# Performance work log

Measured on AMD Instinct MI355X. Metric: run time of the kernel, lower is better.

The kernel has to match this reference:

```python
import jax, jax.numpy as jnp
import numpy as np

EPS = 1e-5

def _layernorm(x, g, b):
    m = jnp.mean(x, axis=-1, keepdims=True)
    v = jnp.var(x, axis=-1, keepdims=True)
    return (x - m) * jax.lax.rsqrt(v + EPS) * g + b

def setup_inputs() -> dict:
    key = jax.random.key(0)
    ks = jax.random.split(key, 8)
    B, N, D, H = 4, 2048, 1024, 16
    F = 2 * D
    s = 0.02
    return {
        "x": jax.random.normal(ks[0], (B, N, D), jnp.float32),
        "mask": jnp.zeros((B, N, N), jnp.float32),
        "Wq": jax.random.normal(ks[1], (D, D), jnp.float32) * s,
        "Wk": jax.random.normal(ks[2], (D, D), jnp.float32) * s,
        "Wv": jax.random.normal(ks[3], (D, D), jnp.float32) * s,
        "Wc": jax.random.normal(ks[4], (D, D), jnp.float32) * s,
        "bc": jnp.zeros((D,), jnp.float32),
        "W1": jax.random.normal(ks[5], (D, F), jnp.float32) * s,
        "b1": jnp.zeros((F,), jnp.float32),
        "W2": jax.random.normal(ks[6], (F, D), jnp.float32) * s,
        "b2": jnp.zeros((D,), jnp.float32),
        "g1": jnp.ones((D,), jnp.float32),
        "be1": jnp.zeros((D,), jnp.float32),
        "g2": jnp.ones((D,), jnp.float32),
        "be2": jnp.zeros((D,), jnp.float32),
    }

def reference(x, mask, Wq, Wk, Wv, Wc, bc, W1, b1, W2, b2, g1, be1, g2, be2):
    B, N, D = x.shape
    H = 16
    Dh = D // H
    scale = 1.0 / np.sqrt(Dh).astype(np.float32)
    # projections -> [B, H, N, Dh]
    def heads(t):
        return t.reshape(B, N, H, Dh).transpose(0, 2, 1, 3)
    q = heads(x @ Wq)
    k = heads(x @ Wk)
    v = heads(x @ Wv)
    score = jnp.einsum('bhnd,bhmd->bhnm', q, k) * scale + mask[:, None, :, :]
    attn = jnp.einsum('bhnm,bhmd->bhnd', jax.nn.softmax(score, axis=-1), v)
    attn = attn.transpose(0, 2, 1, 3).reshape(B, N, D)
    x = x + attn @ Wc + bc
    x = _layernorm(x, g1, be1)
    x = x + jnp.maximum(x @ W1 + b1, 0.0) @ W2 + b2
    x = _layernorm(x, g2, be2)
    return x
```

## Files before the change

kernel.cpp:

```cpp
#include <hip/hip_runtime.h>
#include <hip/hip_bf16.h>


#define DEV __device__ __forceinline__

using s16x8  = __attribute__((ext_vector_type(8))) short;
using f32x4  = __attribute__((ext_vector_type(4))) float;

DEV unsigned short f2bf(float f) {
  unsigned u = __float_as_uint(f);
  u += 0x7fffu + ((u >> 16) & 1u);
  return (unsigned short)(u >> 16);
}
DEV unsigned cvt_pk_bf16(float lo, float hi) {
  unsigned r;
  asm("v_cvt_pk_bf16_f32 %0, %1, %2" : "=v"(r) : "v"(lo), "v"(hi));
  return r;
}
DEV float bf2f(unsigned short b) { return __uint_as_float((unsigned)b << 16); }

typedef __attribute__((address_space(3))) unsigned lds_u32_t;
typedef const __attribute__((address_space(1))) unsigned glb_u32_t;

DEV void gld_lds16(const void* g, void* l) {
  __builtin_amdgcn_global_load_lds((glb_u32_t*)g, (lds_u32_t*)l, 16, 0, 0);
}

template<int RELU, int VOUT>
__global__ __launch_bounds__(512, 2)
void gemm8p(const unsigned short* __restrict__ A, const unsigned short* __restrict__ Bt,
            unsigned short* __restrict__ Cb, const float* __restrict__ bias,
            unsigned short* __restrict__ vtout, int M, int N, int K)
{
  __shared__ unsigned short Sh[2][2][256 * 64];
  const int tid = threadIdx.x;
  const int w = tid >> 6, lane = tid & 63;
  const int g = lane >> 4, q = lane & 15;
  const int wr = w >> 2, wc = w & 3;

  const int nwg  = gridDim.x * gridDim.y;
  const int flat = blockIdx.y * gridDim.x + blockIdx.x;
  const int rm   = (flat & 7) * (nwg >> 3) + (flat >> 3);
  const int m0 = (rm / gridDim.x) * 256, n0 = (rm % gridDim.x) * 256;

  f32x4 acc[8][4] = {};

  const int srow = w * 8 + (lane >> 3);
  const int scol = ((lane & 7) ^ (lane >> 3)) * 8;
  const unsigned short* Ag = A  + (size_t)(m0 + srow) * K + scol;
  const unsigned short* Bg = Bt + (size_t)(n0 + srow) * K + scol;

  auto STG = [&](const unsigned short* Gb, int buf, int ab, int half, int kt) {
    const unsigned short* gs = Gb + (size_t)(half * 128) * K + kt * 64;
    unsigned short* ls = &Sh[buf][ab][(half * 128 + w * 8) * 64];
    gld_lds16(gs, ls);
    gld_lds16(gs + (size_t)64 * K, ls + 64 * 64);
  };
  auto LDA = [&](int buf, int mq, s16x8 af[4][2]) {
#pragma unroll
    for (int mm = 0; mm < 4; ++mm) {
      const unsigned short* rp = &Sh[buf][0][(wr * 128 + mq * 64 + mm * 16 + q) * 64];
#pragma unroll
      for (int kk = 0; kk < 2; ++kk)
        af[mm][kk] = *(const s16x8*)(rp + (((kk * 4 + g) ^ (q & 7)) * 8));
    }
  };
  auto LDB = [&](int buf, int nq, s16x8 bf[2][2]) {
#pragma unroll
    for (int nn = 0; nn < 2; ++nn) {
      const unsigned short* rp = &Sh[buf][1][(wc * 64 + nq * 32 + nn * 16 + q) * 64];
#pragma unroll
      for (int kk = 0; kk < 2; ++kk)
        bf[nn][kk] = *(const s16x8*)(rp + (((kk * 4 + g) ^ (q & 7)) * 8));
    }
  };
  auto MQ = [&](int mq, int nq, const s16x8 af[4][2], const s16x8 bf[2][2]) {
    __builtin_amdgcn_s_setprio(1);
#pragma unroll
    for (int kk = 0; kk < 2; ++kk)
#pragma unroll
      for (int mm = 0; mm < 4; ++mm)
#pragma unroll
        for (int nn = 0; nn < 2; ++nn)
          acc[mq * 4 + mm][nq * 2 + nn] = __builtin_amdgcn_mfma_f32_16x16x32_bf16(
              af[mm][kk], bf[nn][kk], acc[mq * 4 + mm][nq * 2 + nn], 0, 0, 0);
    __builtin_amdgcn_s_setprio(0);
  };
  auto BAR = [&]() { __builtin_amdgcn_sched_barrier(0); __builtin_amdgcn_s_barrier(); };

  STG(Ag, 0, 0, 0, 0); STG(Ag, 0, 0, 1, 0);
  STG(Bg, 0, 1, 0, 0); STG(Bg, 0, 1, 1, 0);

  const int NKT = K >> 6;
  s16x8 af[4][2], bf0[2][2], bf1[2][2];
#pragma unroll 1
  for (int kt = 0; kt < NKT; ++kt) {
    const int b = kt & 1, sb = b ^ 1, kn = kt + 1;
    const bool stg = (kn < NKT);
    if (stg) { STG(Ag, sb, 0, 0, kn); asm volatile("s_waitcnt vmcnt(2)" ::: "memory"); }
    else     {                        asm volatile("s_waitcnt vmcnt(0)" ::: "memory"); }
    BAR();
    LDA(b, 0, af); LDB(b, 0, bf0);
    MQ(0, 0, af, bf0);
    BAR();
    if (stg) STG(Ag, sb, 0, 1, kn);
    LDB(b, 1, bf1);
    MQ(0, 1, af, bf1);
    BAR();
    if (stg) STG(Bg, sb, 1, 0, kn);
    LDA(b, 1, af);
    MQ(1, 0, af, bf0);
    BAR();
    if (stg) STG(Bg, sb, 1, 1, kn);
    MQ(1, 1, af, bf1);
    BAR();
  }

#pragma unroll
  for (int n = 0; n < 4; ++n) {
    const int col = n0 + wc * 64 + n * 16 + q;
    if (VOUT && col >= 2048) {
      const int cv = col - 2048;
#pragma unroll
      for (int m = 0; m < 8; ++m) {
        const int row0 = m0 + wr * 128 + m * 16 + g * 4;
        const int bb = row0 >> 11;
        ushort4 pk;
        pk.x = f2bf(acc[m][n][0]); pk.y = f2bf(acc[m][n][1]);
        pk.z = f2bf(acc[m][n][2]); pk.w = f2bf(acc[m][n][3]);
        *(ushort4*)(vtout + ((size_t)bb * 1024 + cv) * 2048 + (row0 & 2047)) = pk;
      }
    } else {
      const float scl = (VOUT && col < 1024) ? 0.18033688011112042f : 1.0f;
      const float bv = bias ? bias[col] : 0.0f;
#pragma unroll
      for (int m = 0; m < 8; ++m) {
        const int row0 = m0 + wr * 128 + m * 16 + g * 4;
#pragma unroll
        for (int r = 0; r < 4; ++r) {
          float v = acc[m][n][r] * scl + bv;
          if (RELU) v = fmaxf(v, 0.0f);
          Cb[(size_t)(row0 + r) * N + col] = f2bf(v);
        }
      }
    }
  }
}

template<int RELU, int RESID, int OUTF>
__global__ __launch_bounds__(256)
void gemm_bt(const unsigned short* __restrict__ A, const unsigned short* __restrict__ Bt,
             unsigned short* __restrict__ Cb, float* __restrict__ Cf,
             const float* __restrict__ bias, const float* __restrict__ resid,
             const unsigned short* __restrict__ residb,
             int M, int N, int K)
{
  __shared__ unsigned short As[2][4096];
  __shared__ unsigned short Bs[2][4096];
  const int tid  = threadIdx.x;
  const int wave = tid >> 6, lane = tid & 63;
  const int g = lane >> 4, q = lane & 15;

  const int nwg  = gridDim.x * gridDim.y;
  const int flat = blockIdx.y * gridDim.x + blockIdx.x;
  const int rm   = (nwg & 7) ? flat : ((flat & 7) * (nwg >> 3) + (flat >> 3));
  const int m0 = (rm / gridDim.x) * 128, n0 = (rm % gridDim.x) * 128;
  const int wr = wave >> 1, wc = wave & 1;

  f32x4 acc[4][4] = {};

  const int i0 = wave * 512 + lane * 8;
  const int i1 = 2048 + i0;

  auto STAGE = [&](int buf, int kt) {
    gld_lds16(A  + (size_t)(m0 + (i0 >> 5)) * K + kt + (i0 & 31), As[buf] + wave * 512);
    gld_lds16(Bt + (size_t)(n0 + (i0 >> 5)) * K + kt + (i0 & 31), Bs[buf] + wave * 512);
    gld_lds16(A  + (size_t)(m0 + (i1 >> 5)) * K + kt + (i1 & 31), As[buf] + 2048 + wave * 512);
    gld_lds16(Bt + (size_t)(n0 + (i1 >> 5)) * K + kt + (i1 & 31), Bs[buf] + 2048 + wave * 512);
  };

  STAGE(0, 0);
  __syncthreads();
  int cur = 0;
#pragma unroll 1
  for (int kt = 0; kt < K; kt += 32) {
    if (kt + 32 < K) STAGE(cur ^ 1, kt + 32);
    s16x8 a[4], b[4];
#pragma unroll
    for (int m = 0; m < 4; ++m)
      a[m] = *(const s16x8*)(As[cur] + (wr * 64 + m * 16 + q) * 32 + g * 8);
#pragma unroll
    for (int n = 0; n < 4; ++n)
      b[n] = *(const s16x8*)(Bs[cur] + (wc * 64 + n * 16 + q) * 32 + g * 8);
    __builtin_amdgcn_s_setprio(1);
#pragma unroll
    for (int m = 0; m < 4; ++m)
#pragma unroll
      for (int n = 0; n < 4; ++n)
        acc[m][n] = __builtin_amdgcn_mfma_f32_16x16x32_bf16(a[m], b[n], acc[m][n], 0, 0, 0);
    __builtin_amdgcn_s_setprio(0);
    __syncthreads();
    cur ^= 1;
  }

#pragma unroll
  for (int n = 0; n < 4; ++n) {
    const int col = n0 + wc * 64 + n * 16 + q;
    const float bv = bias ? bias[col] : 0.0f;
#pragma unroll
    for (int m = 0; m < 4; ++m) {
      const int row0 = m0 + wr * 64 + m * 16 + g * 4;
#pragma unroll
      for (int r = 0; r < 4; ++r) {
        float v = acc[m][n][r] + bv;
        if (RELU) v = fmaxf(v, 0.0f);
        if (RESID == 1) v += resid[(size_t)(row0 + r) * N + col];
        if (RESID == 2) v += bf2f(residb[(size_t)(row0 + r) * N + col]);
        if (OUTF) Cf[(size_t)(row0 + r) * N + col] = v;
        else      Cb[(size_t)(row0 + r) * N + col] = f2bf(v);
      }
    }
  }
}

__global__ __launch_bounds__(256, 4)
void attn_kernel(const unsigned short* __restrict__ qkv,
                 const unsigned short* __restrict__ vt,
                 const float* __restrict__ mask,
                 unsigned short* __restrict__ outb)
{
  __shared__ unsigned short Ks[2][4096];
  __shared__ unsigned short Vs[2][4096];
  __shared__ unsigned short Pl[4][1024];
  const int tid = threadIdx.x, wave = tid >> 6, lane = tid & 63;
  const int g = lane >> 4, q = lane & 15;

  const int flat = blockIdx.y * 32 + blockIdx.x;
  const int rm   = (flat & 7) * 256 + (flat >> 3);
  const int qt = rm & 31, bh = rm >> 5;
  const int b = bh >> 4, h = bh & 15;
  const int qrow = qt * 64 + wave * 16;
  const size_t tok0 = (size_t)b * 2048;

  const unsigned short* Qp = qkv + (tok0 + qrow + q) * 3072 + h * 64;
  const s16x8 bq0 = *(const s16x8*)(Qp + g * 8);
  const s16x8 bq1 = *(const s16x8*)(Qp + 32 + g * 8);
  const float* Mp = mask + ((size_t)b * 2048 + qrow + q) * 2048 + g * 4;

  const int lr = lane >> 3;
  const int sc = (lane & 7) ^ lr;
  const unsigned short* Kg = qkv + tok0 * 3072 + 1024 + h * 64
                           + (size_t)(wave * 16 + lr) * 3072 + sc * 8;
  const unsigned short* Vg = vt + ((size_t)bh * 64 + wave * 16 + lr) * 2048 + sc * 8;
  unsigned short* KsW = Ks[0] + wave * 1024;
  unsigned short* VsW = Vs[0] + wave * 1024;

  s16x8 ones;
#pragma unroll
  for (int j = 0; j < 8; ++j) ones[j] = (short)0x3F80;

  f32x4 ot[4] = {};
  f32x4 sacc = {};
  f32x4 mk0[4], mk1[4];
  char* Pw = (char*)&Pl[wave][0];
  const float L2E = 1.4426950408889634f;

  gld_lds16(Kg,            KsW);
  gld_lds16(Kg + 8 * 3072, KsW + 512);
  gld_lds16(Vg,            VsW);
  gld_lds16(Vg + 8 * 2048, VsW + 512);
#pragma unroll
  for (int m2 = 0; m2 < 4; ++m2) {
    const f32x4 r = *(const f32x4*)(Mp + m2 * 16);
#pragma unroll
    for (int i = 0; i < 4; ++i) mk0[m2][i] = fmaf(r[i], L2E, -8.0f);
  }
  __syncthreads();

#define ATTN_TILE(BUF, MKC, MKN, STG)                                          \
  {                                                                            \
    f32x4 mu[4];                                                               \
    if (STG) {                                                                 \
      Kg += 64 * 3072; Vg += 64; Mp += 64;                                     \
      gld_lds16(Kg,            KsW + (BUF ^ 1) * 4096);                        \
      gld_lds16(Kg + 8 * 3072, KsW + (BUF ^ 1) * 4096 + 512);                  \
      gld_lds16(Vg,            VsW + (BUF ^ 1) * 4096);                        \
      gld_lds16(Vg + 8 * 2048, VsW + (BUF ^ 1) * 4096 + 512);                  \
      mu[0] = *(const f32x4*)(Mp);      mu[1] = *(const f32x4*)(Mp + 16);      \
      mu[2] = *(const f32x4*)(Mp + 32); mu[3] = *(const f32x4*)(Mp + 48);      \
    }                                                                          \
    __builtin_amdgcn_s_setprio(1);                                             \
    _Pragma("unroll")                                                          \
    for (int m2 = 0; m2 < 4; ++m2) {                                           \
      const unsigned short* kp = Ks[BUF] + (m2 * 16 + q) * 64;                 \
      const s16x8 ak0 = *(const s16x8*)(kp + ((g       ^ (q & 7)) * 8));       \
      const s16x8 ak1 = *(const s16x8*)(kp + (((g + 4) ^ (q & 7)) * 8));       \
      MKC[m2] = __builtin_amdgcn_mfma_f32_16x16x32_bf16(ak0, bq0, MKC[m2], 0, 0, 0); \
      MKC[m2] = __builtin_amdgcn_mfma_f32_16x16x32_bf16(ak1, bq1, MKC[m2], 0, 0, 0); \
    }                                                                          \
    __builtin_amdgcn_s_setprio(0);                                             \
    _Pragma("unroll")                                                          \
    for (int m2 = 0; m2 < 4; ++m2) {                                           \
      MKC[m2][0] = exp2f(MKC[m2][0]); MKC[m2][1] = exp2f(MKC[m2][1]);          \
      MKC[m2][2] = exp2f(MKC[m2][2]); MKC[m2][3] = exp2f(MKC[m2][3]);          \
      const int bir  = m2 * 32 + g * 8;                                        \
      const int addr = q * 128 + (((bir >> 4) ^ (q & 7)) << 4) + (bir & 15);   \
      uint2 pk;                                                                \
      pk.x = cvt_pk_bf16(MKC[m2][0], MKC[m2][1]);                              \
      pk.y = cvt_pk_bf16(MKC[m2][2], MKC[m2][3]);                              \
      *(uint2*)(Pw + addr) = pk;                                               \
    }                                                                          \
    __builtin_amdgcn_s_setprio(1);                                             \
    _Pragma("unroll")                                                          \
    for (int kb = 0; kb < 2; ++kb) {                                           \
      const int blk = (kb * 4 + g) ^ (q & 7);                                  \
      const s16x8 pb = *(const s16x8*)(Pw + q * 128 + blk * 16);               \
      sacc = __builtin_amdgcn_mfma_f32_16x16x32_bf16(ones, pb, sacc, 0, 0, 0); \
      _Pragma("unroll")                                                        \
      for (int mm = 0; mm < 4; ++mm) {                                         \
        const s16x8 av = *(const s16x8*)(Vs[BUF] + (mm * 16 + q) * 64 + blk * 8); \
        ot[mm] = __builtin_amdgcn_mfma_f32_16x16x32_bf16(av, pb, ot[mm], 0, 0, 0); \
      }                                                                        \
    }                                                                          \
    __builtin_amdgcn_s_setprio(0);                                             \
    if (STG) {                                                                 \
      _Pragma("unroll")                                                        \
      for (int m2 = 0; m2 < 4; ++m2) {                                         \
        MKN[m2][0] = fmaf(mu[m2][0], L2E, -8.0f);                              \
        MKN[m2][1] = fmaf(mu[m2][1], L2E, -8.0f);                              \
        MKN[m2][2] = fmaf(mu[m2][2], L2E, -8.0f);                              \
        MKN[m2][3] = fmaf(mu[m2][3], L2E, -8.0f);                              \
      }                                                                        \
    }                                                                          \
    __syncthreads();                                                           \
  }

#pragma unroll 1
  for (int tt = 0; tt < 16; ++tt) {
    ATTN_TILE(0, mk0, mk1, true);
    ATTN_TILE(1, mk1, mk0, (tt < 15));
  }
#undef ATTN_TILE

  const float inv = 1.0f / sacc[0];
#pragma unroll
  for (int mm = 0; mm < 4; ++mm) {
    const int bir  = mm * 32 + g * 8;
    const int addr = q * 128 + (((bir >> 4) ^ (q & 7)) << 4) + (bir & 15);
    uint2 pk;
    pk.x = cvt_pk_bf16(ot[mm][0] * inv, ot[mm][1] * inv);
    pk.y = cvt_pk_bf16(ot[mm][2] * inv, ot[mm][3] * inv);
    *(uint2*)(Pw + addr) = pk;
  }
#pragma unroll
  for (int p = 0; p < 2; ++p) {
    const int c  = p * 64 + lane;
    const int qq = c >> 3, cc = c & 7;
    const int blk = cc ^ (qq & 7);
    const s16x8 vv = *(const s16x8*)(Pw + qq * 128 + blk * 16);
    *(s16x8*)(outb + (tok0 + qrow + qq) * 1024 + h * 64 + cc * 8) = vv;
  }
}

template<int INBF>
__global__ __launch_bounds__(256)
void ln_kernel(const float* __restrict__ inf, const unsigned short* __restrict__ inb,
               float* __restrict__ outf, unsigned short* __restrict__ outb,
               const float* __restrict__ gam, const float* __restrict__ bet)
{
  __shared__ float red[8];
  const int row = blockIdx.x, tid = threadIdx.x;
  f32x4 v;
  if (INBF) {
    const uint2 u = *(const uint2*)(inb + (size_t)row * 1024 + tid * 4);
    v[0] = __uint_as_float(u.x << 16); v[1] = __uint_as_float(u.x & 0xffff0000u);
    v[2] = __uint_as_float(u.y << 16); v[3] = __uint_as_float(u.y & 0xffff0000u);
  } else {
    v = *(const f32x4*)(inf + (size_t)row * 1024 + tid * 4);
  }
  float s  = v[0] + v[1] + v[2] + v[3];
  float ss = v[0]*v[0] + v[1]*v[1] + v[2]*v[2] + v[3]*v[3];
#pragma unroll
  for (int o = 1; o < 64; o <<= 1) { s += __shfl_xor(s, o); ss += __shfl_xor(ss, o); }
  if ((tid & 63) == 0) { red[tid >> 6] = s; red[4 + (tid >> 6)] = ss; }
  __syncthreads();
  s  = red[0] + red[1] + red[2] + red[3];
  ss = red[4] + red[5] + red[6] + red[7];
  const float mean = s * (1.0f / 1024.0f);
  const float var  = ss * (1.0f / 1024.0f) - mean * mean;
  const float rstd = rsqrtf(var + 1e-5f);
  const f32x4 gm = *(const f32x4*)(gam + tid * 4);
  const f32x4 bt = *(const f32x4*)(bet + tid * 4);
  f32x4 o;
#pragma unroll
  for (int j = 0; j < 4; ++j) o[j] = (v[j] - mean) * rstd * gm[j] + bt[j];
  if (outf) *(f32x4*)(outf + (size_t)row * 1024 + tid * 4) = o;
  if (outb) {
    uint2 pk; pk.x = cvt_pk_bf16(o[0], o[1]); pk.y = cvt_pk_bf16(o[2], o[3]);
    *(uint2*)(outb + (size_t)row * 1024 + tid * 4) = pk;
  }
}

__global__ __launch_bounds__(256)
void tcast_kernel(const float* __restrict__ in, unsigned short* __restrict__ out, int R, int C)
{
  __shared__ float t[32][33];
  const int tx = threadIdx.x & 31, ty = threadIdx.x >> 5;
  const int c0 = blockIdx.x * 32, r0 = blockIdx.y * 32;
#pragma unroll
  for (int k = 0; k < 4; ++k)
    t[ty + k * 8][tx] = in[(size_t)(r0 + ty + k * 8) * C + c0 + tx];
  __syncthreads();
#pragma unroll
  for (int k = 0; k < 4; ++k)
    out[(size_t)(c0 + ty + k * 8) * R + r0 + tx] = f2bf(t[tx][ty + k * 8]);
}

__global__ __launch_bounds__(256)
void cast_x_kernel(const float* __restrict__ in, unsigned short* __restrict__ out)
{
  const size_t i = ((size_t)blockIdx.x * 256 + threadIdx.x) * 4;
  const f32x4 v = *(const f32x4*)(in + i);
  uint2 pk; pk.x = cvt_pk_bf16(v[0], v[1]); pk.y = cvt_pk_bf16(v[2], v[3]);
  *(uint2*)(out + i) = pk;
}

extern "C" void kernel_launch(void* const* d_in, const int* in_sizes, int n_in,
                              void* d_out, int out_size, void* d_ws, size_t ws_size,
                              hipStream_t stream)
{
  (void)in_sizes; (void)n_in; (void)out_size; (void)ws_size;
  const float* x   = (const float*)d_in[0];
  const float* msk = (const float*)d_in[1];
  const float* Wq  = (const float*)d_in[2];
  const float* Wk  = (const float*)d_in[3];
  const float* Wv  = (const float*)d_in[4];
  const float* Wc  = (const float*)d_in[5];
  const float* bc  = (const float*)d_in[6];
  const float* W1  = (const float*)d_in[7];
  const float* b1  = (const float*)d_in[8];
  const float* W2  = (const float*)d_in[9];
  const float* b2  = (const float*)d_in[10];
  const float* g1  = (const float*)d_in[11];
  const float* be1 = (const float*)d_in[12];
  const float* g2  = (const float*)d_in[13];
  const float* be2 = (const float*)d_in[14];
  float* out = (float*)d_out;
  char* ws = (char*)d_ws;
  const size_t MB = 1u << 20;
  unsigned short* xb    = (unsigned short*)(ws + 0 * MB);
  unsigned short* wqkvt = (unsigned short*)(ws + 16 * MB);
  unsigned short* wct   = (unsigned short*)(ws + 22 * MB);
  unsigned short* w1t   = (unsigned short*)(ws + 24 * MB);
  unsigned short* w2t   = (unsigned short*)(ws + 28 * MB);
  unsigned short* qkv   = (unsigned short*)(ws + 32 * MB);
  unsigned short* vt    = (unsigned short*)(ws + 80 * MB);
  unsigned short* attnb = (unsigned short*)(ws + 96 * MB);
  unsigned short* y1b   = (unsigned short*)(ws + 112 * MB);
  unsigned short* h1b   = (unsigned short*)(ws + 128 * MB);
  unsigned short* midb  = (unsigned short*)(ws + 32 * MB);
  unsigned short* z2b   = (unsigned short*)(ws + 64 * MB);

  cast_x_kernel<<<8192, 256, 0, stream>>>(x, xb);
  tcast_kernel<<<dim3(32, 32), 256, 0, stream>>>(Wq, wqkvt,               1024, 1024);
  tcast_kernel<<<dim3(32, 32), 256, 0, stream>>>(Wk, wqkvt + 1024 * 1024, 1024, 1024);
  tcast_kernel<<<dim3(32, 32), 256, 0, stream>>>(Wv, wqkvt + 2048 * 1024, 1024, 1024);
  tcast_kernel<<<dim3(32, 32), 256, 0, stream>>>(Wc, wct,                 1024, 1024);
  tcast_kernel<<<dim3(64, 32), 256, 0, stream>>>(W1, w1t,                 1024, 2048);
  tcast_kernel<<<dim3(32, 64), 256, 0, stream>>>(W2, w2t,                 2048, 1024);

  gemm8p<0, 1><<<dim3(12, 32), 512, 0, stream>>>(xb, wqkvt, qkv, nullptr, vt,
                                                 8192, 3072, 1024);
  attn_kernel<<<dim3(32, 64), 256, 0, stream>>>(qkv, vt, msk, attnb);
  gemm_bt<0, 2, 0><<<dim3(8, 64), 256, 0, stream>>>(attnb, wct, y1b, nullptr,
                                                    bc, nullptr, xb, 8192, 1024, 1024);
  ln_kernel<1><<<8192, 256, 0, stream>>>(nullptr, y1b, nullptr, h1b, g1, be1);
  gemm8p<1, 0><<<dim3(8, 32), 512, 0, stream>>>(h1b, w1t, midb, b1, nullptr,
                                                8192, 2048, 1024);
  gemm_bt<0, 2, 0><<<dim3(8, 64), 256, 0, stream>>>(midb, w2t, z2b, nullptr,
                                                    b2, nullptr, h1b, 8192, 1024, 2048);
  ln_kernel<1><<<8192, 256, 0, stream>>>(nullptr, z2b, out, nullptr, g2, be2);
}
```

Baseline: 418.2 us.

## Use 256x128 eight-wave pipelined GEMM for QKV, output and FFN2 projections

Adds a 256x128-tile variant of the eight-wave, double-buffered, swizzled-LDS GEMM that can fuse a residual add. It replaces the simple 128x128 four-wave kernel for the Wc and W2 projections and the 256x256 kernel for the QKV projection. The point is to get the deeper pipelining and larger tiles onto the N=1024 GEMMs while keeping more workgroups, which should improve CU fill: 256 blocks instead of 128 with 256x256 tiles, and 768 instead of 384 for QKV. In exchange there is less B-tile reuse per block than with 256x256 tiles, and more code to maintain.

Measured after the change: 444.0 us. +6.2%, slower.

```diff
diff --git a/kernel.cpp b/kernel.cpp
--- a/kernel.cpp
+++ b/kernel.cpp
@@ -26,40 +26,48 @@
   __builtin_amdgcn_global_load_lds((glb_u32_t*)g, (lds_u32_t*)l, 16, 0, 0);
 }
 
-template<int RELU, int VOUT>
+template<int RESID, int VOUT>
 __global__ __launch_bounds__(512, 2)
-void gemm8p(const unsigned short* __restrict__ A, const unsigned short* __restrict__ Bt,
+void gemm8h(const unsigned short* __restrict__ A, const unsigned short* __restrict__ Bt,
             unsigned short* __restrict__ Cb, const float* __restrict__ bias,
+            const unsigned short* __restrict__ residb,
             unsigned short* __restrict__ vtout, int M, int N, int K)
 {
-  __shared__ unsigned short Sh[2][2][256 * 64];
+  __shared__ unsigned short ShA[2][256 * 64];
+  __shared__ unsigned short ShB[2][128 * 64];
   const int tid = threadIdx.x;
   const int w = tid >> 6, lane = tid & 63;
   const int g = lane >> 4, q = lane & 15;
-  const int wr = w >> 2, wc = w & 3;
+  const int wr = w >> 1, wc = w & 1;
 
   const int nwg  = gridDim.x * gridDim.y;
   const int flat = blockIdx.y * gridDim.x + blockIdx.x;
   const int rm   = (flat & 7) * (nwg >> 3) + (flat >> 3);
-  const int m0 = (rm / gridDim.x) * 256, n0 = (rm % gridDim.x) * 256;
-
-  f32x4 acc[8][4] = {};
+  const int m0 = (rm / gridDim.x) * 256, n0 = (rm % gridDim.x) * 128;
+
+  f32x4 acc[4][4] = {};
 
   const int srow = w * 8 + (lane >> 3);
   const int scol = ((lane & 7) ^ (lane >> 3)) * 8;
   const unsigned short* Ag = A  + (size_t)(m0 + srow) * K + scol;
   const unsigned short* Bg = Bt + (size_t)(n0 + srow) * K + scol;
 
-  auto STG = [&](const unsigned short* Gb, int buf, int ab, int half, int kt) {
-    const unsigned short* gs = Gb + (size_t)(half * 128) * K + kt * 64;
-    unsigned short* ls = &Sh[buf][ab][(half * 128 + w * 8) * 64];
+  auto STGA = [&](int buf, int half, int kt) {
+    const unsigned short* gs = Ag + (size_t)(half * 128) * K + kt * 64;
+    unsigned short* ls = &ShA[buf][(half * 128 + w * 8) * 64];
     gld_lds16(gs, ls);
     gld_lds16(gs + (size_t)64 * K, ls + 64 * 64);
   };
-  auto LDA = [&](int buf, int mq, s16x8 af[4][2]) {
-#pragma unroll
-    for (int mm = 0; mm < 4; ++mm) {
-      const unsigned short* rp = &Sh[buf][0][(wr * 128 + mq * 64 + mm * 16 + q) * 64];
+  auto STGB = [&](int buf, int kt) {
+    const unsigned short* gs = Bg + kt * 64;
+    unsigned short* ls = &ShB[buf][(w * 8) * 64];
+    gld_lds16(gs, ls);
+    gld_lds16(gs + (size_t)64 * K, ls + 64 * 64);
+  };
+  auto LDA = [&](int buf, int mq, s16x8 af[2][2]) {
+#pragma unroll
+    for (int mm = 0; mm < 2; ++mm) {
+      const unsigned short* rp = &ShA[buf][(wr * 64 + mq * 32 + mm * 16 + q) * 64];
 #pragma unroll
       for (int kk = 0; kk < 2; ++kk)
         af[mm][kk] = *(const s16x8*)(rp + (((kk * 4 + g) ^ (q & 7)) * 8));
@@ -68,50 +76,48 @@
   auto LDB = [&](int buf, int nq, s16x8 bf[2][2]) {
 #pragma unroll
     for (int nn = 0; nn < 2; ++nn) {
-      const unsigned short* rp = &Sh[buf][1][(wc * 64 + nq * 32 + nn * 16 + q) * 64];
+      const unsigned short* rp = &ShB[buf][(wc * 64 + nq * 32 + nn * 16 + q) * 64];
 #pragma unroll
       for (int kk = 0; kk < 2; ++kk)
         bf[nn][kk] = *(const s16x8*)(rp + (((kk * 4 + g) ^ (q & 7)) * 8));
     }
   };
-  auto MQ = [&](int mq, int nq, const s16x8 af[4][2], const s16x8 bf[2][2]) {
+  auto MQ = [&](int mq, int nq, const s16x8 af[2][2], const s16x8 bf[2][2]) {
     __builtin_amdgcn_s_setprio(1);
 #pragma unroll
     for (int kk = 0; kk < 2; ++kk)
 #pragma unroll
-      for (int mm = 0; mm < 4; ++mm)
+      for (int mm = 0; mm < 2; ++mm)
 #pragma unroll
         for (int nn = 0; nn < 2; ++nn)
-          acc[mq * 4 + mm][nq * 2 + nn] = __builtin_amdgcn_mfma_f32_16x16x32_bf16(
-              af[mm][kk], bf[nn][kk], acc[mq * 4 + mm][nq * 2 + nn], 0, 0, 0);
+          acc[mq * 2 + mm][nq * 2 + nn] = __builtin_amdgcn_mfma_f32_16x16x32_bf16(
+              af[mm][kk], bf[nn][kk], acc[mq * 2 + mm][nq * 2 + nn], 0, 0, 0);
     __builtin_amdgcn_s_setprio(0);
   };
   auto BAR = [&]() { __builtin_amdgcn_sched_barrier(0); __builtin_amdgcn_s_barrier(); };
 
-  STG(Ag, 0, 0, 0, 0); STG(Ag, 0, 0, 1, 0);
-  STG(Bg, 0, 1, 0, 0); STG(Bg, 0, 1, 1, 0);
+  STGA(0, 0, 0); STGA(0, 1, 0); STGB(0, 0);
 
   const int NKT = K >> 6;
-  s16x8 af[4][2], bf0[2][2], bf1[2][2];
+  s16x8 af[2][2], bf0[2][2], bf1[2][2];
 #pragma unroll 1
   for (int kt = 0; kt < NKT; ++kt) {
     const int b = kt & 1, sb = b ^ 1, kn = kt + 1;
     const bool stg = (kn < NKT);
-    if (stg) { STG(Ag, sb, 0, 0, kn); asm volatile("s_waitcnt vmcnt(2)" ::: "memory"); }
-    else     {                        asm volatile("s_waitcnt vmcnt(0)" ::: "memory"); }
+    if (stg) { STGA(sb, 0, kn); asm volatile("s_waitcnt vmcnt(2)" ::: "memory"); }
+    else     {                  asm volatile("s_waitcnt vmcnt(0)" ::: "memory"); }
     BAR();
     LDA(b, 0, af); LDB(b, 0, bf0);
     MQ(0, 0, af, bf0);
     BAR();
-    if (stg) STG(Ag, sb, 0, 1, kn);
+    if (stg) STGA(sb, 1, kn);
     LDB(b, 1, bf1);
     MQ(0, 1, af, bf1);
     BAR();
-    if (stg) STG(Bg, sb, 1, 0, kn);
+    if (stg) STGB(sb, kn);
     LDA(b, 1, af);
     MQ(1, 0, af, bf0);
     BAR();
-    if (stg) STG(Bg, sb, 1, 1, kn);
     MQ(1, 1, af, bf1);
     BAR();
   }
@@ -122,8 +128,8 @@
     if (VOUT && col >= 2048) {
       const int cv = col - 2048;
 #pragma unroll
-      for (int m = 0; m < 8; ++m) {
-        const int row0 = m0 + wr * 128 + m * 16 + g * 4;
+      for (int m = 0; m < 4; ++m) {
+        const int row0 = m0 + wr * 64 + m * 16 + g * 4;
         const int bb = row0 >> 11;
         ushort4 pk;
         pk.x = f2bf(acc[m][n][0]); pk.y = f2bf(acc[m][n][1]);
@@ -134,12 +140,12 @@
       const float scl = (VOUT && col < 1024) ? 0.18033688011112042f : 1.0f;
       const float bv = bias ? bias[col] : 0.0f;
 #pragma unroll
-      for (int m = 0; m < 8; ++m) {
-        const int row0 = m0 + wr * 128 + m * 16 + g * 4;
+      for (int m = 0; m < 4; ++m) {
+        const int row0 = m0 + wr * 64 + m * 16 + g * 4;
 #pragma unroll
         for (int r = 0; r < 4; ++r) {
-          float v = acc[m][n][r] * scl + bv;
-          if (RELU) v = fmaxf(v, 0.0f);
+          float v = VOUT ? (acc[m][n][r] * scl) : (acc[m][n][r] + bv);
+          if (RESID == 2) v += bf2f(residb[(size_t)(row0 + r) * N + col]);
           Cb[(size_t)(row0 + r) * N + col] = f2bf(v);
         }
       }
@@ -147,60 +153,94 @@
   }
 }
 
-template<int RELU, int RESID, int OUTF>
-__global__ __launch_bounds__(256)
-void gemm_bt(const unsigned short* __restrict__ A, const unsigned short* __restrict__ Bt,
-             unsigned short* __restrict__ Cb, float* __restrict__ Cf,
-             const float* __restrict__ bias, const float* __restrict__ resid,
-             const unsigned short* __restrict__ residb,
-             int M, int N, int K)
-{
-  __shared__ unsigned short As[2][4096];
-  __shared__ unsigned short Bs[2][4096];
-  const int tid  = threadIdx.x;
-  const int wave = tid >> 6, lane = tid & 63;
+template<int RELU>
+__global__ __launch_bounds__(512, 2)
+void gemm8p(const unsigned short* __restrict__ A, const unsigned short* __restrict__ Bt,
+            unsigned short* __restrict__ Cb, const float* __restrict__ bias,
+            int M, int N, int K)
+{
+  __shared__ unsigned short Sh[2][2][256 * 64];
+  const int tid = threadIdx.x;
+  const int w = tid >> 6, lane = tid & 63;
   const int g = lane >> 4, q = lane & 15;
+  const int wr = w >> 2, wc = w & 3;
 
   const int nwg  = gridDim.x * gridDim.y;
   const int flat = blockIdx.y * gridDim.x + blockIdx.x;
-  const int rm   = (nwg & 7) ? flat : ((flat & 7) * (nwg >> 3) + (flat >> 3));
-  const int m0 = (rm / gridDim.x) * 128, n0 = (rm % gridDim.x) * 128;
-  const int wr = wave >> 1, wc = wave & 1;
-
-  f32x4 acc[4][4] = {};
-
-  const int i0 = wave * 512 + lane * 8;
-  const int i1 = 2048 + i0;
-
-  auto STAGE = [&](int buf, int kt) {
-    gld_lds16(A  + (size_t)(m0 + (i0 >> 5)) * K + kt + (i0 & 31), As[buf] + wave * 512);
-    gld_lds16(Bt + (size_t)(n0 + (i0 >> 5)) * K + kt + (i0 & 31), Bs[buf] + wave * 512);
-    gld_lds16(A  + (size_t)(m0 + (i1 >> 5)) * K + kt + (i1 & 31), As[buf] + 2048 + wave * 512);
-    gld_lds16(Bt + (size_t)(n0 + (i1 >> 5)) * K + kt + (i1 & 31), Bs[buf] + 2048 + wave * 512);
-  };
-
-  STAGE(0, 0);
-  __syncthreads();
-  int cur = 0;
+  const int rm   = (flat & 7) * (nwg >> 3) + (flat >> 3);
+  const int m0 = (rm / gridDim.x) * 256, n0 = (rm % gridDim.x) * 256;
+
+  f32x4 acc[8][4] = {};
+
+  const int srow = w * 8 + (lane >> 3);
+  const int scol = ((lane & 7) ^ (lane >> 3)) * 8;
+  const unsigned short* Ag = A  + (size_t)(m0 + srow) * K + scol;
+  const unsigned short* Bg = Bt + (size_t)(n0 + srow) * K + scol;
+
+  auto STG = [&](const unsigned short* Gb, int buf, int ab, int half, int kt) {
+    const unsigned short* gs = Gb + (size_t)(half * 128) * K + kt * 64;
+    unsigned short* ls = &Sh[buf][ab][(half * 128 + w * 8) * 64];
+    gld_lds16(gs, ls);
+    gld_lds16(gs + (size_t)64 * K, ls + 64 * 64);
+  };
+  auto LDA = [&](int buf, int mq, s16x8 af[4][2]) {
+#pragma unroll
+    for (int mm = 0; mm < 4; ++mm) {
+      const unsigned short* rp = &Sh[buf][0][(wr * 128 + mq * 64 + mm * 16 + q) * 64];
+#pragma unroll
+      for (int kk = 0; kk < 2; ++kk)
+        af[mm][kk] = *(const s16x8*)(rp + (((kk * 4 + g) ^ (q & 7)) * 8));
+    }
+  };
+  auto LDB = [&](int buf, int nq, s16x8 bf[2][2]) {
+#pragma unroll
+    for (int nn = 0; nn < 2; ++nn) {
+      const unsigned short* rp = &Sh[buf][1][(wc * 64 + nq * 32 + nn * 16 + q) * 64];
+#pragma unroll
+      for (int kk = 0; kk < 2; ++kk)
+        bf[nn][kk] = *(const s16x8*)(rp + (((kk * 4 + g) ^ (q & 7)) * 8));
+    }
+  };
+  auto MQ = [&](int mq, int nq, const s16x8 af[4][2], const s16x8 bf[2][2]) {
+    __builtin_amdgcn_s_setprio(1);
+#pragma unroll
+    for (int kk = 0; kk < 2; ++kk)
+#pragma unroll
+      for (int mm = 0; mm < 4; ++mm)
+#pragma unroll
+        for (int nn = 0; nn < 2; ++nn)
+          acc[mq * 4 + mm][nq * 2 + nn] = __builtin_amdgcn_mfma_f32_16x16x32_bf16(
+              af[mm][kk], bf[nn][kk], acc[mq * 4 + mm][nq * 2 + nn], 0, 0, 0);
+    __builtin_amdgcn_s_setprio(0);
+  };
+  auto BAR = [&]() { __builtin_amdgcn_sched_barrier(0); __builtin_amdgcn_s_barrier(); };
+
+  STG(Ag, 0, 0, 0, 0); STG(Ag, 0, 0, 1, 0);
+  STG(Bg, 0, 1, 0, 0); STG(Bg, 0, 1, 1, 0);
+
+  const int NKT = K >> 6;
+  s16x8 af[4][2], bf0[2][2], bf1[2][2];
 #pragma unroll 1
-  for (int kt = 0; kt < K; kt += 32) {
-    if (kt + 32 < K) STAGE(cur ^ 1, kt + 32);
-    s16x8 a[4], b[4];
-#pragma unroll
-    for (int m = 0; m < 4; ++m)
-      a[m] = *(const s16x8*)(As[cur] + (wr * 64 + m * 16 + q) * 32 + g * 8);
-#pragma unroll
-    for (int n = 0; n < 4; ++n)
-      b[n] = *(const s16x8*)(Bs[cur] + (wc * 64 + n * 16 + q) * 32 + g * 8);
-    __builtin_amdgcn_s_setprio(1);
-#pragma unroll
-    for (int m = 0; m < 4; ++m)
-#pragma unroll
-      for (int n = 0; n < 4; ++n)
-        acc[m][n] = __builtin_amdgcn_mfma_f32_16x16x32_bf16(a[m], b[n], acc[m][n], 0, 0, 0);
-    __builtin_amdgcn_s_setprio(0);
-    __syncthreads();
-    cur ^= 1;
+  for (int kt = 0; kt < NKT; ++kt) {
+    const int b = kt & 1, sb = b ^ 1, kn = kt + 1;
+    const bool stg = (kn < NKT);
+    if (stg) { STG(Ag, sb, 0, 0, kn); asm volatile("s_waitcnt vmcnt(2)" ::: "memory"); }
+    else     {                        asm volatile("s_waitcnt vmcnt(0)" ::: "memory"); }
+    BAR();
+    LDA(b, 0, af); LDB(b, 0, bf0);
+    MQ(0, 0, af, bf0);
+    BAR();
+    if (stg) STG(Ag, sb, 0, 1, kn);
+    LDB(b, 1, bf1);
+    MQ(0, 1, af, bf1);
+    BAR();
+    if (stg) STG(Bg, sb, 1, 0, kn);
+    LDA(b, 1, af);
+    MQ(1, 0, af, bf0);
+    BAR();
+    if (stg) STG(Bg, sb, 1, 1, kn);
+    MQ(1, 1, af, bf1);
+    BAR();
   }
 
 #pragma unroll
@@ -208,16 +248,13 @@
     const int col = n0 + wc * 64 + n * 16 + q;
     const float bv = bias ? bias[col] : 0.0f;
 #pragma unroll
-    for (int m = 0; m < 4; ++m) {
-      const int row0 = m0 + wr * 64 + m * 16 + g * 4;
+    for (int m = 0; m < 8; ++m) {
+      const int row0 = m0 + wr * 128 + m * 16 + g * 4;
 #pragma unroll
       for (int r = 0; r < 4; ++r) {
         float v = acc[m][n][r] + bv;
         if (RELU) v = fmaxf(v, 0.0f);
-        if (RESID == 1) v += resid[(size_t)(row0 + r) * N + col];
-        if (RESID == 2) v += bf2f(residb[(size_t)(row0 + r) * N + col]);
-        if (OUTF) Cf[(size_t)(row0 + r) * N + col] = v;
-        else      Cb[(size_t)(row0 + r) * N + col] = f2bf(v);
+        Cb[(size_t)(row0 + r) * N + col] = f2bf(v);
       }
     }
   }
@@ -469,15 +506,14 @@
   tcast_kernel<<<dim3(64, 32), 256, 0, stream>>>(W1, w1t,                 1024, 2048);
   tcast_kernel<<<dim3(32, 64), 256, 0, stream>>>(W2, w2t,                 2048, 1024);
 
-  gemm8p<0, 1><<<dim3(12, 32), 512, 0, stream>>>(xb, wqkvt, qkv, nullptr, vt,
-                                                 8192, 3072, 1024);
+  gemm8h<0, 1><<<dim3(24, 32), 512, 0, stream>>>(xb, wqkvt, qkv, nullptr,
+                                                 nullptr, vt, 8192, 3072, 1024);
   attn_kernel<<<dim3(32, 64), 256, 0, stream>>>(qkv, vt, msk, attnb);
-  gemm_bt<0, 2, 0><<<dim3(8, 64), 256, 0, stream>>>(attnb, wct, y1b, nullptr,
-                                                    bc, nullptr, xb, 8192, 1024, 1024);
+  gemm8h<2, 0><<<dim3(8, 32), 512, 0, stream>>>(attnb, wct, y1b, bc,
+                                                xb, nullptr, 8192, 1024, 1024);
   ln_kernel<1><<<8192, 256, 0, stream>>>(nullptr, y1b, nullptr, h1b, g1, be1);
-  gemm8p<1, 0><<<dim3(8, 32), 512, 0, stream>>>(h1b, w1t, midb, b1, nullptr,
-                                                8192, 2048, 1024);
-  gemm_bt<0, 2, 0><<<dim3(8, 64), 256, 0, stream>>>(midb, w2t, z2b, nullptr,
-                                                    b2, nullptr, h1b, 8192, 1024, 2048);
+  gemm8p<1><<<dim3(8, 32), 512, 0, stream>>>(h1b, w1t, midb, b1, 8192, 2048, 1024);
+  gemm8h<2, 0><<<dim3(8, 32), 512, 0, stream>>>(midb, w2t, z2b, b2,
+                                                h1b, nullptr, 8192, 1024, 2048);
   ln_kernel<1><<<8192, 256, 0, stream>>>(nullptr, z2b, out, nullptr, g2, be2);
 }
```
